# Kernel optimization log

Hardware: AMD Instinct MI355X
Metric: run time of the kernel (lower is better)

## Reference

```python
import jax, jax.numpy as jnp
import numpy as np

N_NODES = 50000
N_EDGES = 1600000
IN_CH = 128
HID = 128
OUT_CH = 6
NUM_GRAPHS = 512


def _lin_params(key, fan_in, fan_out):
    k1, k2 = jax.random.split(key)
    bound = 1.0 / np.sqrt(fan_in)
    W = jax.random.uniform(k1, (fan_in, fan_out), minval=-bound, maxval=bound, dtype=jnp.float32)
    b = jax.random.uniform(k2, (fan_out,), minval=-bound, maxval=bound, dtype=jnp.float32)
    return W, b


def setup_inputs() -> dict:
    key = jax.random.key(0)
    ks = jax.random.split(key, 10)
    x = jax.random.normal(ks[0], (N_NODES, IN_CH), dtype=jnp.float32)
    edge_index = jax.random.randint(ks[1], (2, N_EDGES), 0, N_NODES, dtype=jnp.int64)
    batch = jnp.sort(jax.random.randint(ks[2], (N_NODES,), 0, NUM_GRAPHS, dtype=jnp.int64))
    W1a, b1a = _lin_params(ks[3], IN_CH, HID)
    W1b, b1b = _lin_params(ks[4], HID, HID)
    W2a, b2a = _lin_params(ks[5], HID, HID)
    W2b, b2b = _lin_params(ks[6], HID, HID)
    Wf1, bf1 = _lin_params(ks[7], HID, HID)
    Wf2, bf2 = _lin_params(ks[8], HID, OUT_CH)
    return {"x": x, "edge_index": edge_index, "batch": batch,
            "W1a": W1a, "b1a": b1a, "W1b": W1b, "b1b": b1b,
            "W2a": W2a, "b2a": b2a, "W2b": W2b, "b2b": b2b,
            "Wf1": Wf1, "bf1": bf1, "Wf2": Wf2, "bf2": bf2}


def _gin_conv(x, src, dst, Wa, ba, Wb, bb):
    # aggregate: sum of source-node features into target nodes (eps = 0)
    agg = jax.ops.segment_sum(x[src], dst, num_segments=N_NODES)
    h = x + agg  # (1 + eps) * x + sum_neighbors
    h = jax.nn.relu(h @ Wa + ba) @ Wb + bb  # 2-layer MLP (nn1/nn2)
    return h


def reference(x, edge_index, batch, W1a, b1a, W1b, b1b, W2a, b2a, W2b, b2b, Wf1, bf1, Wf2, bf2):
    src, dst = edge_index[0], edge_index[1]
    h = jax.nn.relu(_gin_conv(x, src, dst, W1a, b1a, W1b, b1b))
    h = jax.nn.relu(_gin_conv(h, src, dst, W2a, b2a, W2b, b2b))
    # global mean pool over graph ids
    sums = jax.ops.segment_sum(h, batch, num_segments=NUM_GRAPHS)  # [G, HID]
    counts = jax.ops.segment_sum(jnp.ones((h.shape[0],), h.dtype), batch, num_segments=NUM_GRAPHS)
    pooled = sums / jnp.maximum(counts, 1.0)[:, None]
    out = jax.nn.relu(pooled @ Wf1 + bf1) @ Wf2 + bf2  # [G, 6]
    return jax.nn.sigmoid(out)
```

## Files before the change

### kernel.cpp

```cpp
#include <hip/hip_runtime.h>

typedef unsigned short u16;
typedef unsigned int u32;

#define N_NODES 50000
#define N_EDGES 1600000
#define CH 128
#define CHW 64
#define NG 512
#define CAP 128
#define PAD 136
#define NBINS 196
#define BINCAP 12288
#define NSCAT 512
#define ECHUNK 3125

typedef __bf16 bf16x8 __attribute__((ext_vector_type(8)));
typedef float f32x4 __attribute__((ext_vector_type(4)));

#define OFF_DEG 0ull
#define OFF_BUCKET 200192ull
#define OFF_XB 13000192ull
#define OFF_HSUM 25800192ull
#define OFF_H1 38600192ull
#define OFF_POOL 51400192ull
#define OFF_GS 51662336ull
#define OFF_GE 51664384ull
#define OFF_WT 51666432ull
#define OFF_BC 51797504ull
#define OFF_WF1 51799552ull
#define OFF_BF1 51865088ull
#define OFF_WF2 51865600ull
#define OFF_BF2 51868672ull
#define OFF_BCUR 51868928ull

__device__ __forceinline__ float bflo(u32 v) { return __builtin_bit_cast(float, v << 16); }
__device__ __forceinline__ float bfhi(u32 v) { return __builtin_bit_cast(float, v & 0xffff0000u); }
__device__ __forceinline__ float bf2f(u16 v) { return __builtin_bit_cast(float, ((u32)v) << 16); }
__device__ __forceinline__ u16 f2bf(float f) {
    u32 x = __builtin_bit_cast(u32, f);
    x += 0x7fffu + ((x >> 16) & 1u);
    return (u16)(x >> 16);
}
__device__ __forceinline__ u32 pack2(float a, float b) {
    return (u32)f2bf(a) | ((u32)f2bf(b) << 16);
}
__device__ __forceinline__ bool probe_bf16(u32 w0) {
    u32 ex = (w0 >> 7) & 0xFFu;
    bool ok = ((w0 & 0x7FFFu) == 0u) || (ex >= 0x70u && ex <= 0x8Fu);
    return __popcll(__ballot(ok)) >= 48;
}
__device__ __forceinline__ float loadf(const void* p, int i, bool isbf) {
    return isbf ? bf2f(((const u16*)p)[i]) : ((const float*)p)[i];
}

__global__ __launch_bounds__(256) void prep_params(char* ws,
                                                   const void* W0, const void* W1,
                                                   const void* W2, const void* W3,
                                                   const void* b0, const void* b1,
                                                   const void* b2, const void* b3,
                                                   const void* Wf1, const void* bf1,
                                                   const void* Wf2, const void* bf2) {
    int lane = threadIdx.x & 63;
    bool isbf = probe_bf16(((const u32*)W0)[lane]);
    int idx = blockIdx.x * 256 + threadIdx.x;
    u16* Wt = (u16*)(ws + OFF_WT);
    float* bc = (float*)(ws + OFF_BC);
    float* Wf1c = (float*)(ws + OFF_WF1);
    float* bf1c = (float*)(ws + OFF_BF1);
    float* Wf2c = (float*)(ws + OFF_WF2);
    float* bf2c = (float*)(ws + OFF_BF2);
    if (idx < 65536) {
        int j = idx >> 14, r = idx & 16383;
        int n = r >> 7, k = r & 127;
        const void* src = (j == 0) ? W0 : (j == 1) ? W1 : (j == 2) ? W2 : W3;
        float v = loadf(src, k * 128 + n, isbf);
        Wt[idx] = f2bf(v);
    } else if (idx < 66048) {
        int r = idx - 65536, j = r >> 7, c = r & 127;
        const void* src = (j == 0) ? b0 : (j == 1) ? b1 : (j == 2) ? b2 : b3;
        bc[r] = loadf(src, c, isbf);
    } else if (idx < 82432) {
        Wf1c[idx - 66048] = loadf(Wf1, idx - 66048, isbf);
    } else if (idx < 82560) {
        bf1c[idx - 82432] = loadf(bf1, idx - 82432, isbf);
    } else if (idx < 83328) {
        Wf2c[idx - 82560] = loadf(Wf2, idx - 82560, isbf);
    } else if (idx < 83334) {
        bf2c[idx - 83328] = loadf(bf2, idx - 83328, isbf);
    }
}

__global__ __launch_bounds__(256) void cvt_x(const u32* __restrict__ x, u32* __restrict__ xb) {
    int lane = threadIdx.x & 63;
    bool isbf = probe_bf16(x[lane]);
    int i = blockIdx.x * 256 + threadIdx.x;
    if (i >= N_NODES * CHW) return;
    if (isbf) {
        xb[i] = x[i];
    } else {
        float2 v = ((const float2*)x)[i];
        xb[i] = pack2(v.x, v.y);
    }
}

__global__ __launch_bounds__(256) void edge_scatter(const int* __restrict__ ei,
                                                    int* __restrict__ binCursor,
                                                    u32* __restrict__ binned) {
    __shared__ u32 lhist[256];
    __shared__ u32 lbase[256];
    __shared__ u32 lcur[256];
    int tid = threadIdx.x, wg = blockIdx.x;
    int lane = tid & 63;
    u32 hiw = ((const u32*)ei)[2 * lane + 1];
    bool i64 = __popcll(__ballot(hiw == 0u)) >= 48;
    int e0 = wg * ECHUNK;
    lhist[tid] = 0; lcur[tid] = 0;
    __syncthreads();
    for (int e = e0 + tid; e < e0 + ECHUNK; e += 256) {
        int d = i64 ? ei[2 * N_EDGES + 2 * e] : ei[N_EDGES + e];
        atomicAdd(&lhist[d >> 8], 1u);
    }
    __syncthreads();
    u32 c = lhist[tid];
    if (c) lbase[tid] = (u32)atomicAdd(&binCursor[tid], (int)c);
    __syncthreads();
    for (int e = e0 + tid; e < e0 + ECHUNK; e += 256) {
        int s, d;
        if (i64) { s = ei[2 * e]; d = ei[2 * N_EDGES + 2 * e]; }
        else     { s = ei[e];     d = ei[N_EDGES + e]; }
        int b = d >> 8;
        u32 p = atomicAdd(&lcur[b], 1u);
        binned[(size_t)b * BINCAP + lbase[b] + p] = ((u32)d << 16) | (u32)s;
    }
}

__global__ __launch_bounds__(256) void fill_from_binned(const int* __restrict__ binCursor,
                                                        const u32* __restrict__ binned,
                                                        int* __restrict__ deg,
                                                        u16* __restrict__ bucket) {
    __shared__ u32 ldeg[256];
    int tid = threadIdx.x, b = blockIdx.x;
    int cnt = binCursor[b];
    ldeg[tid] = 0;
    __syncthreads();
    const u32* bp = binned + (size_t)b * BINCAP;
    for (int i = tid; i < cnt; i += 256) {
        u32 w = bp[i];
        u32 dl = (w >> 16) & 255u;
        u32 pos = atomicAdd(&ldeg[dl], 1u);
        if (pos < CAP) bucket[(size_t)(w >> 16) * CAP + pos] = (u16)(w & 0xFFFFu);
    }
    __syncthreads();
    int node = b * 256 + tid;
    if (node < N_NODES) deg[node] = (int)ldeg[tid];
}

__global__ __launch_bounds__(256) void agg_kernel(const u32* __restrict__ h,
                                                  const int* __restrict__ deg,
                                                  const u16* __restrict__ bucket,
                                                  u32* __restrict__ out) {
    int w = threadIdx.x >> 6, lane = threadIdx.x & 63;
    int node = blockIdx.x * 4 + w;
    if (node >= N_NODES) return;
    int sub = lane >> 4, q = lane & 15;
    const uint4* h4 = (const uint4*)h;
    float acc[8];
    {
        uint4 sv = make_uint4(0u, 0u, 0u, 0u);
        if (sub == 0) sv = h4[(size_t)node * 16 + q];
        acc[0] = bflo(sv.x); acc[1] = bfhi(sv.x);
        acc[2] = bflo(sv.y); acc[3] = bfhi(sv.y);
        acc[4] = bflo(sv.z); acc[5] = bfhi(sv.z);
        acc[6] = bflo(sv.w); acc[7] = bfhi(sv.w);
    }
    int d = deg[node];
    d = d > CAP ? CAP : d;
    const u32* bkw = (const u32*)(bucket + (size_t)node * CAP);
    const u32 sh = (u32)(sub & 1) * 16u;
    const int widx = sub >> 1;
    int j = 0;
    for (; j + 16 <= d; j += 16) {
        int base = j >> 1;
        u32 wd0 = bkw[base + widx];
        u32 wd1 = bkw[base + 2 + widx];
        u32 wd2 = bkw[base + 4 + widx];
        u32 wd3 = bkw[base + 6 + widx];
        uint4 v0 = h4[(size_t)((wd0 >> sh) & 0xFFFFu) * 16 + q];
        uint4 v1 = h4[(size_t)((wd1 >> sh) & 0xFFFFu) * 16 + q];
        uint4 v2 = h4[(size_t)((wd2 >> sh) & 0xFFFFu) * 16 + q];
        uint4 v3 = h4[(size_t)((wd3 >> sh) & 0xFFFFu) * 16 + q];
        acc[0] += bflo(v0.x) + bflo(v1.x) + bflo(v2.x) + bflo(v3.x);
        acc[1] += bfhi(v0.x) + bfhi(v1.x) + bfhi(v2.x) + bfhi(v3.x);
        acc[2] += bflo(v0.y) + bflo(v1.y) + bflo(v2.y) + bflo(v3.y);
        acc[3] += bfhi(v0.y) + bfhi(v1.y) + bfhi(v2.y) + bfhi(v3.y);
        acc[4] += bflo(v0.z) + bflo(v1.z) + bflo(v2.z) + bflo(v3.z);
        acc[5] += bfhi(v0.z) + bfhi(v1.z) + bfhi(v2.z) + bfhi(v3.z);
        acc[6] += bflo(v0.w) + bflo(v1.w) + bflo(v2.w) + bflo(v3.w);
        acc[7] += bfhi(v0.w) + bfhi(v1.w) + bfhi(v2.w) + bfhi(v3.w);
    }
    for (; j + 4 <= d; j += 4) {
        u32 wd = bkw[(j >> 1) + widx];
        uint4 v = h4[(size_t)((wd >> sh) & 0xFFFFu) * 16 + q];
        acc[0] += bflo(v.x); acc[1] += bfhi(v.x);
        acc[2] += bflo(v.y); acc[3] += bfhi(v.y);
        acc[4] += bflo(v.z); acc[5] += bfhi(v.z);
        acc[6] += bflo(v.w); acc[7] += bfhi(v.w);
    }
    if (j + sub < d) {
        int e = j + sub;
        u32 wd = bkw[e >> 1];
        u32 id = (wd >> ((u32)(e & 1) * 16u)) & 0xFFFFu;
        uint4 v = h4[(size_t)id * 16 + q];
        acc[0] += bflo(v.x); acc[1] += bfhi(v.x);
        acc[2] += bflo(v.y); acc[3] += bfhi(v.y);
        acc[4] += bflo(v.z); acc[5] += bfhi(v.z);
        acc[6] += bflo(v.w); acc[7] += bfhi(v.w);
    }
#pragma unroll
    for (int c = 0; c < 8; ++c) {
        acc[c] += __shfl_xor(acc[c], 16, 64);
        acc[c] += __shfl_xor(acc[c], 32, 64);
    }
    if (sub == 0) {
        uint4 o;
        o.x = pack2(acc[0], acc[1]);
        o.y = pack2(acc[2], acc[3]);
        o.z = pack2(acc[4], acc[5]);
        o.w = pack2(acc[6], acc[7]);
        ((uint4*)out)[(size_t)node * 16 + q] = o;
    }
}

__global__ __launch_bounds__(256) void mlp_kernel(const u16* __restrict__ in,
                                                  const u16* __restrict__ Wta,
                                                  const float* __restrict__ ba,
                                                  const u16* __restrict__ Wtb,
                                                  const float* __restrict__ bb,
                                                  u16* __restrict__ out,
                                                  int nrows) {
    __shared__ __align__(16) u16 Wlds[128 * PAD];
    __shared__ __align__(16) u16 tlds[64 * PAD];
    const int tid = threadIdx.x;
    const int w = tid >> 6;
    const int lane = tid & 63;
    const int n16 = lane & 15;
    const int quad = lane >> 4;
    const int row0 = blockIdx.x * 64 + w * 16;
    const bool active = row0 < nrows;

    {
        const uint4* wsrc = (const uint4*)Wta;
#pragma unroll
        for (int it = 0; it < 8; ++it) {
            int idx = tid + it * 256;
            int n = idx >> 4, c = idx & 15;
            *(uint4*)&Wlds[n * PAD + c * 8] = wsrc[idx];
        }
    }
    __syncthreads();

    f32x4 acc[8];
    bf16x8 afrag[4];
    if (active) {
        const u16* rowp = in + (size_t)(row0 + n16) * CH + quad * 8;
#pragma unroll
        for (int ks = 0; ks < 4; ++ks)
            afrag[ks] = *(const bf16x8*)(rowp + ks * 32);
#pragma unroll
        for (int ct = 0; ct < 8; ++ct) {
            f32x4 a = {0.f, 0.f, 0.f, 0.f};
#pragma unroll
            for (int ks = 0; ks < 4; ++ks) {
                bf16x8 b = *(const bf16x8*)&Wlds[(u32)(ct * 16 + n16) * PAD + ks * 32 + quad * 8];
                a = __builtin_amdgcn_mfma_f32_16x16x32_bf16(afrag[ks], b, a, 0, 0, 0);
            }
            acc[ct] = a;
        }
#pragma unroll
        for (int ct = 0; ct < 8; ++ct) {
            float bv = ba[ct * 16 + n16];
#pragma unroll
            for (int r = 0; r < 4; ++r) {
                float v = fmaxf(acc[ct][r] + bv, 0.f);
                tlds[(w * 16 + quad * 4 + r) * PAD + ct * 16 + n16] = f2bf(v);
            }
        }
    }
    __syncthreads();
    {
        const uint4* wsrc = (const uint4*)Wtb;
#pragma unroll
        for (int it = 0; it < 8; ++it) {
            int idx = tid + it * 256;
            int n = idx >> 4, c = idx & 15;
            *(uint4*)&Wlds[n * PAD + c * 8] = wsrc[idx];
        }
    }
    __syncthreads();

    if (active) {
#pragma unroll
        for (int ks = 0; ks < 4; ++ks)
            afrag[ks] = *(const bf16x8*)&tlds[(u32)(w * 16 + n16) * PAD + ks * 32 + quad * 8];
#pragma unroll
        for (int ct = 0; ct < 8; ++ct) {
            f32x4 a = {0.f, 0.f, 0.f, 0.f};
#pragma unroll
            for (int ks = 0; ks < 4; ++ks) {
                bf16x8 b = *(const bf16x8*)&Wlds[(u32)(ct * 16 + n16) * PAD + ks * 32 + quad * 8];
                a = __builtin_amdgcn_mfma_f32_16x16x32_bf16(afrag[ks], b, a, 0, 0, 0);
            }
            acc[ct] = a;
        }
#pragma unroll
        for (int ct = 0; ct < 8; ++ct) {
            float bv = bb[ct * 16 + n16];
#pragma unroll
            for (int r = 0; r < 4; ++r) {
                float v = fmaxf(acc[ct][r] + bv, 0.f);
                tlds[(w * 16 + quad * 4 + r) * PAD + ct * 16 + n16] = f2bf(v);
            }
        }
        u32* outw = (u32*)out;
        for (int r = 0; r < 16; ++r) {
            u32 v = *(const u32*)&tlds[(w * 16 + r) * PAD + lane * 2];
            outw[(size_t)(row0 + r) * CHW + lane] = v;
        }
    }
}

__global__ __launch_bounds__(256) void graph_bounds(const int* __restrict__ batch,
                                                    int* __restrict__ gstart,
                                                    int* __restrict__ gend) {
    int lane = threadIdx.x & 63;
    u32 hiw = ((const u32*)batch)[2 * (12500 + lane) + 1];
    bool i64 = __popcll(__ballot(hiw == 0u)) >= 48;
    int i = blockIdx.x * 256 + threadIdx.x;
    if (i >= N_NODES) return;
    int g = i64 ? batch[2 * i] : batch[i];
    atomicMin(&gstart[g], i);
    atomicMax(&gend[g], i + 1);
}

__global__ __launch_bounds__(256) void pool_kernel(const u32* __restrict__ h,
                                                   const int* __restrict__ gstart,
                                                   const int* __restrict__ gend,
                                                   float* __restrict__ pooled) {
    int w = threadIdx.x >> 6, lane = threadIdx.x & 63;
    int g = blockIdx.x * 4 + w;
    if (g >= NG) return;
    int s = gstart[g], e = gend[g];
    float ax = 0.f, ay = 0.f;
    if (s < e) {
        int i = s;
        for (; i + 4 <= e; i += 4) {
            u32 v0 = h[(size_t)(i + 0) * CHW + lane];
            u32 v1 = h[(size_t)(i + 1) * CHW + lane];
            u32 v2 = h[(size_t)(i + 2) * CHW + lane];
            u32 v3 = h[(size_t)(i + 3) * CHW + lane];
            ax += bflo(v0) + bflo(v1) + bflo(v2) + bflo(v3);
            ay += bfhi(v0) + bfhi(v1) + bfhi(v2) + bfhi(v3);
        }
        for (; i < e; ++i) {
            u32 v = h[(size_t)i * CHW + lane];
            ax += bflo(v);
            ay += bfhi(v);
        }
    }
    float inv = 1.f / (float)((s < e) ? (e - s) : 1);
    ((float2*)pooled)[(size_t)g * CHW + lane] = make_float2(ax * inv, ay * inv);
}

__global__ __launch_bounds__(256) void final_kernel(const float* __restrict__ pooled,
                                                    const float* __restrict__ Wf1,
                                                    const float* __restrict__ bf1,
                                                    const float* __restrict__ Wf2,
                                                    const float* __restrict__ bf2v,
                                                    float* __restrict__ out) {
    __shared__ float rowb[4][128];
    __shared__ float tb[4][128];
    int w = threadIdx.x >> 6, lane = threadIdx.x & 63;
    int g = blockIdx.x * 4 + w;
    float2 rv = ((const float2*)pooled)[(size_t)g * CHW + lane];
    rowb[w][2 * lane] = rv.x;
    rowb[w][2 * lane + 1] = rv.y;
    __syncthreads();
#pragma unroll
    for (int jj = 0; jj < 2; ++jj) {
        int j = lane + jj * 64;
        float a = bf1[j];
        for (int k = 0; k < 128; ++k) a += rowb[w][k] * Wf1[k * 128 + j];
        tb[w][j] = fmaxf(a, 0.f);
    }
    __syncthreads();
    if (lane < 6) {
        float a = bf2v[lane];
        for (int k = 0; k < 128; ++k) a += tb[w][k] * Wf2[k * 6 + lane];
        out[g * 6 + lane] = 1.f / (1.f + __expf(-a));
    }
}

extern "C" void kernel_launch(void* const* d_in, const int* in_sizes, int n_in,
                              void* d_out, int out_size, void* d_ws, size_t ws_size,
                              hipStream_t stream) {
    const u32* x = (const u32*)d_in[0];
    const int* ei = (const int*)d_in[1];
    const int* batch = (const int*)d_in[2];
    float* out = (float*)d_out;

    char* ws = (char*)d_ws;
    int* deg = (int*)(ws + OFF_DEG);
    u16* bucket = (u16*)(ws + OFF_BUCKET);
    u32* XB = (u32*)(ws + OFF_XB);
    u32* HSUM = (u32*)(ws + OFF_HSUM);
    u32* H1 = (u32*)(ws + OFF_H1);
    float* pooled = (float*)(ws + OFF_POOL);
    int* gstart = (int*)(ws + OFF_GS);
    int* gend = (int*)(ws + OFF_GE);
    u16* Wt = (u16*)(ws + OFF_WT);
    float* bc = (float*)(ws + OFF_BC);
    float* Wf1c = (float*)(ws + OFF_WF1);
    float* bf1c = (float*)(ws + OFF_BF1);
    float* Wf2c = (float*)(ws + OFF_WF2);
    float* bf2c = (float*)(ws + OFF_BF2);
    int* binCursor = (int*)(ws + OFF_BCUR);
    u32* binned = HSUM;

    hipMemsetAsync(binCursor, 0, 1024, stream);
    hipMemsetAsync(gstart, 0x7F, NG * 4, stream);
    hipMemsetAsync(gend, 0, NG * 4, stream);

    prep_params<<<326, 256, 0, stream>>>(ws,
        d_in[3], d_in[5], d_in[7], d_in[9],
        d_in[4], d_in[6], d_in[8], d_in[10],
        d_in[11], d_in[12], d_in[13], d_in[14]);
    cvt_x<<<(N_NODES * CHW) / 256, 256, 0, stream>>>(x, XB);
    edge_scatter<<<NSCAT, 256, 0, stream>>>(ei, binCursor, binned);
    fill_from_binned<<<NBINS, 256, 0, stream>>>(binCursor, binned, deg, bucket);
    graph_bounds<<<(N_NODES + 255) / 256, 256, 0, stream>>>(batch, gstart, gend);

    agg_kernel<<<(N_NODES + 3) / 4, 256, 0, stream>>>(XB, deg, bucket, HSUM);
    mlp_kernel<<<(N_NODES + 63) / 64, 256, 0, stream>>>((const u16*)HSUM, Wt, bc,
                                                        Wt + 16384, bc + 128, (u16*)H1, N_NODES);
    agg_kernel<<<(N_NODES + 3) / 4, 256, 0, stream>>>(H1, deg, bucket, HSUM);
    mlp_kernel<<<(N_NODES + 63) / 64, 256, 0, stream>>>((const u16*)HSUM, Wt + 32768, bc + 256,
                                                        Wt + 49152, bc + 384, (u16*)XB, N_NODES);
    pool_kernel<<<(NG + 3) / 4, 256, 0, stream>>>(XB, gstart, gend, pooled);
    final_kernel<<<NG / 4, 256, 0, stream>>>(pooled, Wf1c, bf1c, Wf2c, bf2c, out);
}
```

Measured before the change: 329.9 us.

## Fold memsets and graph bounds into prep kernels, stash edges, widen gathers

The three hipMemsetAsync calls are replaced by zero/fill work inside prep_params, and graph_bounds is merged into the x-conversion kernel, which removes several launches. The weight transpose now goes through a padded LDS tile so global reads and writes are coalesced. edge_scatter packs each edge into an LDS stash during the histogram pass, so the edge index array is read once instead of twice. The aggregation loop gains a 32-neighbour unrolled stage for more loads in flight. The pool kernel uses 16-byte loads with four row groups per wave and a shuffle reduction. The cost is more register and LDS use per kernel, which may lower occupancy.

```diff
diff --git a/kernel.cpp b/kernel.cpp
--- a/kernel.cpp
+++ b/kernel.cpp
@@ -61,46 +61,83 @@
                                                    const void* b2, const void* b3,
                                                    const void* Wf1, const void* bf1,
                                                    const void* Wf2, const void* bf2) {
-    int lane = threadIdx.x & 63;
+    __shared__ float tile[128 * 129];
+    int tid = threadIdx.x;
+    int lane = tid & 63;
     bool isbf = probe_bf16(((const u32*)W0)[lane]);
-    int idx = blockIdx.x * 256 + threadIdx.x;
-    u16* Wt = (u16*)(ws + OFF_WT);
+    int b = blockIdx.x;
+    if (b < 4) {
+        const void* src = (b == 0) ? W0 : (b == 1) ? W1 : (b == 2) ? W2 : W3;
+#pragma unroll 4
+        for (int it = 0; it < 64; ++it) {
+            int idx = it * 256 + tid;
+            int k = idx >> 7, n = idx & 127;
+            tile[k * 129 + n] = loadf(src, idx, isbf);
+        }
+        __syncthreads();
+        u16* Wt = (u16*)(ws + OFF_WT) + b * 16384;
+#pragma unroll 4
+        for (int it = 0; it < 64; ++it) {
+            int o = it * 256 + tid;
+            int n = o >> 7, k = o & 127;
+            Wt[o] = f2bf(tile[k * 129 + n]);
+        }
+        return;
+    }
+    int idx = (b - 4) * 256 + tid;
     float* bc = (float*)(ws + OFF_BC);
     float* Wf1c = (float*)(ws + OFF_WF1);
     float* bf1c = (float*)(ws + OFF_BF1);
     float* Wf2c = (float*)(ws + OFF_WF2);
     float* bf2c = (float*)(ws + OFF_BF2);
-    if (idx < 65536) {
-        int j = idx >> 14, r = idx & 16383;
-        int n = r >> 7, k = r & 127;
-        const void* src = (j == 0) ? W0 : (j == 1) ? W1 : (j == 2) ? W2 : W3;
-        float v = loadf(src, k * 128 + n, isbf);
-        Wt[idx] = f2bf(v);
-    } else if (idx < 66048) {
-        int r = idx - 65536, j = r >> 7, c = r & 127;
+    int* binCursor = (int*)(ws + OFF_BCUR);
+    int* gstart = (int*)(ws + OFF_GS);
+    int* gend = (int*)(ws + OFF_GE);
+    if (idx < 512) {
+        int j = idx >> 7, c = idx & 127;
         const void* src = (j == 0) ? b0 : (j == 1) ? b1 : (j == 2) ? b2 : b3;
-        bc[r] = loadf(src, c, isbf);
-    } else if (idx < 82432) {
-        Wf1c[idx - 66048] = loadf(Wf1, idx - 66048, isbf);
-    } else if (idx < 82560) {
-        bf1c[idx - 82432] = loadf(bf1, idx - 82432, isbf);
-    } else if (idx < 83328) {
-        Wf2c[idx - 82560] = loadf(Wf2, idx - 82560, isbf);
-    } else if (idx < 83334) {
-        bf2c[idx - 83328] = loadf(bf2, idx - 83328, isbf);
-    }
-}
-
-__global__ __launch_bounds__(256) void cvt_x(const u32* __restrict__ x, u32* __restrict__ xb) {
+        bc[idx] = loadf(src, c, isbf);
+    } else if (idx < 16896) {
+        Wf1c[idx - 512] = loadf(Wf1, idx - 512, isbf);
+    } else if (idx < 17024) {
+        bf1c[idx - 16896] = loadf(bf1, idx - 16896, isbf);
+    } else if (idx < 17792) {
+        Wf2c[idx - 17024] = loadf(Wf2, idx - 17024, isbf);
+    } else if (idx < 17798) {
+        bf2c[idx - 17792] = loadf(bf2, idx - 17792, isbf);
+    } else if (idx < 18054) {
+        binCursor[idx - 17798] = 0;
+    } else if (idx < 18566) {
+        gstart[idx - 18054] = 0x7F7F7F7F;
+    } else if (idx < 19078) {
+        gend[idx - 18566] = 0;
+    }
+}
+
+__global__ __launch_bounds__(256) void cvt_gb(const u32* __restrict__ x, u32* __restrict__ xb,
+                                              const int* __restrict__ batch,
+                                              int* __restrict__ gstart,
+                                              int* __restrict__ gend) {
     int lane = threadIdx.x & 63;
     bool isbf = probe_bf16(x[lane]);
     int i = blockIdx.x * 256 + threadIdx.x;
-    if (i >= N_NODES * CHW) return;
-    if (isbf) {
-        xb[i] = x[i];
-    } else {
-        float2 v = ((const float2*)x)[i];
-        xb[i] = pack2(v.x, v.y);
+    if (i < N_NODES * CHW) {
+        if (isbf) {
+            xb[i] = x[i];
+        } else {
+            float2 v = ((const float2*)x)[i];
+            xb[i] = pack2(v.x, v.y);
+        }
+    }
+    if (blockIdx.x < 196) {
+        u32 hiw = ((const u32*)batch)[2 * (12500 + lane) + 1];
+        bool i64 = __popcll(__ballot(hiw == 0u)) >= 48;
+        int n = blockIdx.x * 256 + threadIdx.x;
+        if (n < N_NODES) {
+            int g = i64 ? batch[2 * n] : batch[n];
+            atomicMin(&gstart[g], n);
+            atomicMax(&gend[g], n + 1);
+        }
     }
 }
 
@@ -110,6 +147,7 @@
     __shared__ u32 lhist[256];
     __shared__ u32 lbase[256];
     __shared__ u32 lcur[256];
+    __shared__ u32 stash[ECHUNK];
     int tid = threadIdx.x, wg = blockIdx.x;
     int lane = tid & 63;
     u32 hiw = ((const u32*)ei)[2 * lane + 1];
@@ -117,21 +155,23 @@
     int e0 = wg * ECHUNK;
     lhist[tid] = 0; lcur[tid] = 0;
     __syncthreads();
-    for (int e = e0 + tid; e < e0 + ECHUNK; e += 256) {
-        int d = i64 ? ei[2 * N_EDGES + 2 * e] : ei[N_EDGES + e];
-        atomicAdd(&lhist[d >> 8], 1u);
-    }
-    __syncthreads();
-    u32 c = lhist[tid];
-    if (c) lbase[tid] = (u32)atomicAdd(&binCursor[tid], (int)c);
-    __syncthreads();
-    for (int e = e0 + tid; e < e0 + ECHUNK; e += 256) {
+    for (int li = tid; li < ECHUNK; li += 256) {
+        int e = e0 + li;
         int s, d;
         if (i64) { s = ei[2 * e]; d = ei[2 * N_EDGES + 2 * e]; }
         else     { s = ei[e];     d = ei[N_EDGES + e]; }
-        int b = d >> 8;
+        stash[li] = ((u32)d << 16) | (u32)s;
+        atomicAdd(&lhist[d >> 8], 1u);
+    }
+    __syncthreads();
+    u32 c = lhist[tid];
+    if (c) lbase[tid] = (u32)atomicAdd(&binCursor[tid], (int)c);
+    __syncthreads();
+    for (int li = tid; li < ECHUNK; li += 256) {
+        u32 w = stash[li];
+        int b = (int)(w >> 24);
         u32 p = atomicAdd(&lcur[b], 1u);
-        binned[(size_t)b * BINCAP + lbase[b] + p] = ((u32)d << 16) | (u32)s;
+        binned[(size_t)b * BINCAP + lbase[b] + p] = w;
     }
 }
 
@@ -180,6 +220,41 @@
     const u32 sh = (u32)(sub & 1) * 16u;
     const int widx = sub >> 1;
     int j = 0;
+    for (; j + 32 <= d; j += 32) {
+        int base = j >> 1;
+        u32 wd0 = bkw[base + widx];
+        u32 wd1 = bkw[base + 2 + widx];
+        u32 wd2 = bkw[base + 4 + widx];
+        u32 wd3 = bkw[base + 6 + widx];
+        u32 wd4 = bkw[base + 8 + widx];
+        u32 wd5 = bkw[base + 10 + widx];
+        u32 wd6 = bkw[base + 12 + widx];
+        u32 wd7 = bkw[base + 14 + widx];
+        uint4 v0 = h4[(size_t)((wd0 >> sh) & 0xFFFFu) * 16 + q];
+        uint4 v1 = h4[(size_t)((wd1 >> sh) & 0xFFFFu) * 16 + q];
+        uint4 v2 = h4[(size_t)((wd2 >> sh) & 0xFFFFu) * 16 + q];
+        uint4 v3 = h4[(size_t)((wd3 >> sh) & 0xFFFFu) * 16 + q];
+        uint4 v4 = h4[(size_t)((wd4 >> sh) & 0xFFFFu) * 16 + q];
+        uint4 v5 = h4[(size_t)((wd5 >> sh) & 0xFFFFu) * 16 + q];
+        uint4 v6 = h4[(size_t)((wd6 >> sh) & 0xFFFFu) * 16 + q];
+        uint4 v7 = h4[(size_t)((wd7 >> sh) & 0xFFFFu) * 16 + q];
+        acc[0] += bflo(v0.x) + bflo(v1.x) + bflo(v2.x) + bflo(v3.x)
+                + bflo(v4.x) + bflo(v5.x) + bflo(v6.x) + bflo(v7.x);
+        acc[1] += bfhi(v0.x) + bfhi(v1.x) + bfhi(v2.x) + bfhi(v3.x)
+                + bfhi(v4.x) + bfhi(v5.x) + bfhi(v6.x) + bfhi(v7.x);
+        acc[2] += bflo(v0.y) + bflo(v1.y) + bflo(v2.y) + bflo(v3.y)
+                + bflo(v4.y) + bflo(v5.y) + bflo(v6.y) + bflo(v7.y);
+        acc[3] += bfhi(v0.y) + bfhi(v1.y) + bfhi(v2.y) + bfhi(v3.y)
+                + bfhi(v4.y) + bfhi(v5.y) + bfhi(v6.y) + bfhi(v7.y);
+        acc[4] += bflo(v0.z) + bflo(v1.z) + bflo(v2.z) + bflo(v3.z)
+                + bflo(v4.z) + bflo(v5.z) + bflo(v6.z) + bflo(v7.z);
+        acc[5] += bfhi(v0.z) + bfhi(v1.z) + bfhi(v2.z) + bfhi(v3.z)
+                + bfhi(v4.z) + bfhi(v5.z) + bfhi(v6.z) + bfhi(v7.z);
+        acc[6] += bflo(v0.w) + bflo(v1.w) + bflo(v2.w) + bflo(v3.w)
+                + bflo(v4.w) + bflo(v5.w) + bflo(v6.w) + bflo(v7.w);
+        acc[7] += bfhi(v0.w) + bfhi(v1.w) + bfhi(v2.w) + bfhi(v3.w)
+                + bfhi(v4.w) + bfhi(v5.w) + bfhi(v6.w) + bfhi(v7.w);
+    }
     for (; j + 16 <= d; j += 16) {
         int base = j >> 1;
         u32 wd0 = bkw[base + widx];
@@ -330,19 +405,6 @@
     }
 }
 
-__global__ __launch_bounds__(256) void graph_bounds(const int* __restrict__ batch,
-                                                    int* __restrict__ gstart,
-                                                    int* __restrict__ gend) {
-    int lane = threadIdx.x & 63;
-    u32 hiw = ((const u32*)batch)[2 * (12500 + lane) + 1];
-    bool i64 = __popcll(__ballot(hiw == 0u)) >= 48;
-    int i = blockIdx.x * 256 + threadIdx.x;
-    if (i >= N_NODES) return;
-    int g = i64 ? batch[2 * i] : batch[i];
-    atomicMin(&gstart[g], i);
-    atomicMax(&gend[g], i + 1);
-}
-
 __global__ __launch_bounds__(256) void pool_kernel(const u32* __restrict__ h,
                                                    const int* __restrict__ gstart,
                                                    const int* __restrict__ gend,
@@ -350,26 +412,38 @@
     int w = threadIdx.x >> 6, lane = threadIdx.x & 63;
     int g = blockIdx.x * 4 + w;
     if (g >= NG) return;
+    int sub = lane >> 4, q = lane & 15;
     int s = gstart[g], e = gend[g];
-    float ax = 0.f, ay = 0.f;
-    if (s < e) {
-        int i = s;
-        for (; i + 4 <= e; i += 4) {
-            u32 v0 = h[(size_t)(i + 0) * CHW + lane];
-            u32 v1 = h[(size_t)(i + 1) * CHW + lane];
-            u32 v2 = h[(size_t)(i + 2) * CHW + lane];
-            u32 v3 = h[(size_t)(i + 3) * CHW + lane];
-            ax += bflo(v0) + bflo(v1) + bflo(v2) + bflo(v3);
-            ay += bfhi(v0) + bfhi(v1) + bfhi(v2) + bfhi(v3);
-        }
-        for (; i < e; ++i) {
-            u32 v = h[(size_t)i * CHW + lane];
-            ax += bflo(v);
-            ay += bfhi(v);
-        }
-    }
-    float inv = 1.f / (float)((s < e) ? (e - s) : 1);
-    ((float2*)pooled)[(size_t)g * CHW + lane] = make_float2(ax * inv, ay * inv);
+    const uint4* h4 = (const uint4*)h;
+    float acc[8] = {0.f, 0.f, 0.f, 0.f, 0.f, 0.f, 0.f, 0.f};
+    int i = s + sub;
+    for (; i + 4 < e; i += 8) {
+        uint4 v0 = h4[(size_t)i * 16 + q];
+        uint4 v1 = h4[(size_t)(i + 4) * 16 + q];
+        acc[0] += bflo(v0.x) + bflo(v1.x); acc[1] += bfhi(v0.x) + bfhi(v1.x);
+        acc[2] += bflo(v0.y) + bflo(v1.y); acc[3] += bfhi(v0.y) + bfhi(v1.y);
+        acc[4] += bflo(v0.z) + bflo(v1.z); acc[5] += bfhi(v0.z) + bfhi(v1.z);
+        acc[6] += bflo(v0.w) + bflo(v1.w); acc[7] += bfhi(v0.w) + bfhi(v1.w);
+    }
+    for (; i < e; i += 4) {
+        uint4 v = h4[(size_t)i * 16 + q];
+        acc[0] += bflo(v.x); acc[1] += bfhi(v.x);
+        acc[2] += bflo(v.y); acc[3] += bfhi(v.y);
+        acc[4] += bflo(v.z); acc[5] += bfhi(v.z);
+        acc[6] += bflo(v.w); acc[7] += bfhi(v.w);
+    }
+#pragma unroll
+    for (int c = 0; c < 8; ++c) {
+        acc[c] += __shfl_xor(acc[c], 16, 64);
+        acc[c] += __shfl_xor(acc[c], 32, 64);
+    }
+    if (sub == 0) {
+        float inv = 1.f / (float)((s < e) ? (e - s) : 1);
+        float4 a0 = make_float4(acc[0] * inv, acc[1] * inv, acc[2] * inv, acc[3] * inv);
+        float4 a1 = make_float4(acc[4] * inv, acc[5] * inv, acc[6] * inv, acc[7] * inv);
+        ((float4*)pooled)[(size_t)g * 32 + q * 2] = a0;
+        ((float4*)pooled)[(size_t)g * 32 + q * 2 + 1] = a1;
+    }
 }
 
 __global__ __launch_bounds__(256) void final_kernel(const float* __restrict__ pooled,
@@ -427,18 +501,13 @@
     int* binCursor = (int*)(ws + OFF_BCUR);
     u32* binned = HSUM;
 
-    hipMemsetAsync(binCursor, 0, 1024, stream);
-    hipMemsetAsync(gstart, 0x7F, NG * 4, stream);
-    hipMemsetAsync(gend, 0, NG * 4, stream);
-
-    prep_params<<<326, 256, 0, stream>>>(ws,
+    prep_params<<<79, 256, 0, stream>>>(ws,
         d_in[3], d_in[5], d_in[7], d_in[9],
         d_in[4], d_in[6], d_in[8], d_in[10],
         d_in[11], d_in[12], d_in[13], d_in[14]);
-    cvt_x<<<(N_NODES * CHW) / 256, 256, 0, stream>>>(x, XB);
+    cvt_gb<<<(N_NODES * CHW) / 256, 256, 0, stream>>>(x, XB, batch, gstart, gend);
     edge_scatter<<<NSCAT, 256, 0, stream>>>(ei, binCursor, binned);
     fill_from_binned<<<NBINS, 256, 0, stream>>>(binCursor, binned, deg, bucket);
-    graph_bounds<<<(N_NODES + 255) / 256, 256, 0, stream>>>(batch, gstart, gend);
 
     agg_kernel<<<(N_NODES + 3) / 4, 256, 0, stream>>>(XB, deg, bucket, HSUM);
     mlp_kernel<<<(N_NODES + 63) / 64, 256, 0, stream>>>((const u16*)HSUM, Wt, bc,
```

After: 340.3 us. 3.2% more time.
